# Optimization experiments

Measured on AMD Instinct MI355X. Metric: run time of the kernel, lower is better.

Reference implementation:

```python
import jax, jax.numpy as jnp
import numpy as np

H, D_MODEL, TOPK = 8, 512, 32
D_K = D_MODEL // H


def setup_inputs() -> dict:
    key = jax.random.key(0)
    ks = jax.random.split(key, 12)
    B, LQ, LM = 8, 1024, 4096
    s = 1.0 / np.sqrt(D_MODEL)
    inp = {
        "query": jax.random.normal(ks[0], (B, LQ, D_MODEL), jnp.float32),
        "key": jax.random.normal(ks[1], (B, LM, D_MODEL), jnp.float32),
        "value": jax.random.normal(ks[2], (B, LM, D_MODEL), jnp.float32),
        "Wq": jax.random.normal(ks[3], (D_MODEL, D_MODEL), jnp.float32) * s,
        "bq": jax.random.normal(ks[4], (D_MODEL,), jnp.float32) * s,
        "Wk": jax.random.normal(ks[5], (D_MODEL, D_MODEL), jnp.float32) * s,
        "bk": jax.random.normal(ks[6], (D_MODEL,), jnp.float32) * s,
        "Wv": jax.random.normal(ks[7], (D_MODEL, D_MODEL), jnp.float32) * s,
        "bv": jax.random.normal(ks[8], (D_MODEL,), jnp.float32) * s,
        "Wo": jax.random.normal(ks[9], (D_MODEL, D_MODEL), jnp.float32) * s,
        "bo": jax.random.normal(ks[10], (D_MODEL,), jnp.float32) * s,
    }
    return inp


def reference(query, key, value, Wq, bq, Wk, bk, Wv, bv, Wo, bo):
    B, LQ, _ = query.shape
    LM = key.shape[1]
    # torch Linear: x @ W.T + b
    q = (query @ Wq.T + bq).reshape(B, LQ, H, D_K).transpose(0, 2, 1, 3)  # [B,H,LQ,Dk]
    k = (key @ Wk.T + bk).reshape(B, LM, H, D_K).transpose(0, 2, 1, 3)    # [B,H,LM,Dk]
    v = (value @ Wv.T + bv).reshape(B, LM, H, D_K).transpose(0, 2, 1, 3)  # [B,H,LM,Dk]

    scores = jnp.einsum("bhqd,bhmd->bhqm", q, k) / np.sqrt(D_K)          # [B,H,LQ,LM]
    sel_scores, idx = jax.lax.top_k(scores, TOPK)                          # [B,H,LQ,TOPK]
    # gather selected values: [B,H,LQ,TOPK,Dk]
    sel_v = jnp.take_along_axis(v[:, :, None, :, :], idx[..., None], axis=3)
    p_attn = jax.nn.softmax(sel_scores, axis=-1)                           # dropout: eval mode
    x = jnp.einsum("bhqt,bhqtd->bhqd", p_attn, sel_v)                      # [B,H,LQ,Dk]
    x = x.transpose(0, 2, 1, 3).reshape(B, LQ, H * D_K)
    return x @ Wo.T + bo
```

## Files before the change

kernel.cpp:

```cpp
#include <hip/hip_runtime.h>
#include <math.h>

#define DEV static __device__ __forceinline__

DEV void load8(const float* p, float* v) {
    float4 a = *(const float4*)p;
    float4 b = *(const float4*)(p + 4);
    v[0] = a.x; v[1] = a.y; v[2] = a.z; v[3] = a.w;
    v[4] = b.x; v[5] = b.y; v[6] = b.z; v[7] = b.w;
}

DEV void gemm_body(const float* __restrict__ A, const float* __restrict__ W,
                   const float* __restrict__ bias, float* __restrict__ C,
                   int bm, int bn, int tid,
                   float (*As)[68], float (*Bs)[68])
{
    constexpr int BK = 32, NK = 512;
    const int tx = tid & 15, ty = tid >> 4;
    const int lr = tid >> 2, lk = (tid & 3) * 8;
    float acc[4][4] = {};

    for (int k0 = 0; k0 < NK; k0 += BK) {
        float va[8], vb[8];
        load8(A + (size_t)(bm + lr) * NK + k0 + lk, va);
        load8(W + (size_t)(bn + lr) * NK + k0 + lk, vb);
#pragma unroll
        for (int i = 0; i < 8; ++i) { As[lk + i][lr] = va[i]; Bs[lk + i][lr] = vb[i]; }
        __syncthreads();
#pragma unroll
        for (int kk = 0; kk < BK; ++kk) {
            float4 a4 = *(const float4*)&As[kk][ty * 4];
            float4 b4 = *(const float4*)&Bs[kk][tx * 4];
            float a[4] = {a4.x, a4.y, a4.z, a4.w};
            float b[4] = {b4.x, b4.y, b4.z, b4.w};
#pragma unroll
            for (int i = 0; i < 4; ++i)
#pragma unroll
                for (int j = 0; j < 4; ++j)
                    acc[i][j] = fmaf(a[i], b[j], acc[i][j]);
        }
        __syncthreads();
    }

    float4 bvv4 = *(const float4*)&bias[bn + tx * 4];
    float bvv[4] = {bvv4.x, bvv4.y, bvv4.z, bvv4.w};
#pragma unroll
    for (int i = 0; i < 4; ++i) {
        size_t row = (size_t)(bm + ty * 4 + i) * NK + bn + tx * 4;
        float4 o;
        o.x = acc[i][0] + bvv[0];
        o.y = acc[i][1] + bvv[1];
        o.z = acc[i][2] + bvv[2];
        o.w = acc[i][3] + bvv[3];
        *(float4*)&C[row] = o;
    }
}

__global__ __launch_bounds__(256) void gemm_nt512(
    const float* __restrict__ A, const float* __restrict__ W,
    const float* __restrict__ bias, float* __restrict__ C)
{
    __shared__ float As[32][68];
    __shared__ float Bs[32][68];
    gemm_body(A, W, bias, C, blockIdx.y * 64, blockIdx.x * 64, threadIdx.x, As, Bs);
}

__global__ __launch_bounds__(256) void gemm_qkv(
    const float* __restrict__ Aq, const float* __restrict__ Ak, const float* __restrict__ Av,
    const float* __restrict__ Wq, const float* __restrict__ Wk, const float* __restrict__ Wv,
    const float* __restrict__ bq, const float* __restrict__ bk, const float* __restrict__ bv,
    float* __restrict__ Cq, float* __restrict__ Ck, float* __restrict__ Cv)
{
    __shared__ float As[32][68];
    __shared__ float Bs[32][68];
    int yb = blockIdx.y;
    const float *A, *W, *bias; float* C; int bm;
    if (yb < 128)      { A = Aq; W = Wq; bias = bq; C = Cq; bm = yb * 64; }
    else if (yb < 640) { A = Ak; W = Wk; bias = bk; C = Ck; bm = (yb - 128) * 64; }
    else               { A = Av; W = Wv; bias = bv; C = Cv; bm = (yb - 640) * 64; }
    gemm_body(A, W, bias, C, bm, blockIdx.x * 64, threadIdx.x, As, Bs);
}

__global__ __launch_bounds__(256) void topk_attn_fused(
    const float* __restrict__ Qf, const float* __restrict__ Kf,
    const float* __restrict__ Vp, float* __restrict__ Xp,
    unsigned short* __restrict__ gbuf)
{
    constexpr int LQ = 1024, LM = 4096, DK = 64, D = 512, QT = 32, MT = 256, TK = 32, T = 24;
    constexpr int CAP = 624;
    __shared__ __align__(16) char smem[69632 + 8704 + 128];
    float (*ks)[68]   = (float (*)[68])(smem);
    float (*sc)[264]  = (float (*)[264])(smem + 34816);
    float (*wsel)[33] = (float (*)[33])(smem);
    int   (*isel)[33] = (int   (*)[33])(smem + 4224);
    float (*qs)[68]   = (float (*)[68])(smem + 69632);
    int*  cnt         = (int*)(smem + 69632 + 8704);

    const int tid  = threadIdx.x;
    const int lane = tid & 63;
    const int w    = tid >> 6;
    const int g    = lane >> 3, j = lane & 7;
    const int r    = 8 * w + g;
    const int qt = blockIdx.x, h = blockIdx.y, b = blockIdx.z;

    const size_t bb = ((size_t)(((b * 8) + h) * 32 + qt) * 32 + r) * CAP;

    {
        int rr = tid >> 3, d0 = (tid & 7) * 8;
        const float* src = Qf + ((size_t)(b * LQ + qt * QT + rr) * D + h * DK + d0);
        float4 a = *(const float4*)src;
        float4 c = *(const float4*)(src + 4);
        *(float4*)&qs[rr][d0]     = a;
        *(float4*)&qs[rr][d0 + 4] = c;
    }
    if (tid < 32) cnt[tid] = 0;

    float s0 = -INFINITY, s1 = -INFINITY, s2 = -INFINITY, s3 = -INFINITY;
    float tau = -INFINITY;

    const int qy = tid >> 5, tx = tid & 31;
    const int srr = tid >> 2, sd0 = (tid & 3) * 16;
    __syncthreads();

#pragma unroll 1
    for (int mc = 0; mc < LM; mc += MT) {
#pragma unroll
        for (int p = 0; p < 4; ++p) {
            const float* src = Kf + ((size_t)(b * LM + mc + 64 * p + srr) * D + h * DK + sd0);
#pragma unroll
            for (int i2 = 0; i2 < 16; i2 += 4)
                *(float4*)&ks[64 * p + srr][sd0 + i2] = *(const float4*)(src + i2);
        }
        __syncthreads();

        float acc[4][8] = {};
#pragma unroll 2
        for (int dc = 0; dc < DK; dc += 4) {
            float4 qa[4], kb[8];
#pragma unroll
            for (int i = 0; i < 4; ++i) qa[i] = *(const float4*)&qs[qy + 8 * i][dc];
#pragma unroll
            for (int jj = 0; jj < 8; ++jj) kb[jj] = *(const float4*)&ks[tx + 32 * jj][dc];
#pragma unroll
            for (int i = 0; i < 4; ++i)
#pragma unroll
                for (int jj = 0; jj < 8; ++jj) {
                    acc[i][jj] = fmaf(qa[i].x, kb[jj].x, acc[i][jj]);
                    acc[i][jj] = fmaf(qa[i].y, kb[jj].y, acc[i][jj]);
                    acc[i][jj] = fmaf(qa[i].z, kb[jj].z, acc[i][jj]);
                    acc[i][jj] = fmaf(qa[i].w, kb[jj].w, acc[i][jj]);
                }
        }
        __syncthreads();

#pragma unroll
        for (int i = 0; i < 4; ++i)
#pragma unroll
            for (int jj = 0; jj < 8; ++jj)
                sc[qy + 8 * i][tx + 32 * jj] = acc[i][jj] * 0.125f;
        __syncthreads();

#pragma unroll 8
        for (int c = 0; c < 32; ++c) {
            float v = sc[r][8 * c + j];
            if (v > s3) {
                if (v > s0)      { s3 = s2; s2 = s1; s1 = s0; s0 = v; }
                else if (v > s1) { s3 = s2; s2 = s1; s1 = v; }
                else if (v > s2) { s3 = s2; s2 = v; }
                else             { s3 = v; }
            }
            if (v > tau) {
                int pos = atomicAdd(&cnt[r], 1);
                if (pos < CAP) gbuf[bb + pos] = (unsigned short)(mc + 8 * c + j);
            }
            if ((c & 7) == 7) {
                float t4 = s3;
                t4 = fminf(t4, __shfl_xor(t4, 1));
                t4 = fminf(t4, __shfl_xor(t4, 2));
                t4 = fminf(t4, __shfl_xor(t4, 4));
                tau = t4;
            }
        }
        __syncthreads();
    }

    const int nc = min(cnt[r], CAP);
    float bv[T]; int bi[T];
#pragma unroll
    for (int t = 0; t < T; ++t) { bv[t] = -INFINITY; bi[t] = 0; }
    float curmin = -INFINITY; int minpos = 0, minidx = 0;

#pragma unroll 1
    for (int p = j; p < nc; p += 8) {
        int idx = gbuf[bb + p];
        const float* krow = Kf + ((size_t)(b * LM + idx) * D + h * DK);
        float a = 0.0f;
#pragma unroll
        for (int d = 0; d < DK; d += 4) {
            float4 k4 = *(const float4*)(krow + d);
            float4 q4 = *(const float4*)&qs[r][d];
            a = fmaf(q4.x, k4.x, a);
            a = fmaf(q4.y, k4.y, a);
            a = fmaf(q4.z, k4.z, a);
            a = fmaf(q4.w, k4.w, a);
        }
        float v = a * 0.125f;

        bool take = (v > curmin) || (v == curmin && idx < minidx);
        if (take) {
#pragma unroll
            for (int t = 0; t < T; ++t)
                if (t == minpos) { bv[t] = v; bi[t] = idx; }
            float mv = bv[0]; int mp = 0, mi = bi[0];
#pragma unroll
            for (int t = 1; t < T; ++t)
                if (bv[t] < mv || (bv[t] == mv && bi[t] > mi)) { mv = bv[t]; mp = t; mi = bi[t]; }
            curmin = mv; minpos = mp; minidx = mi;
        }
    }

    unsigned cons = 0;
    float m0 = 0.0f;
    double sum_part = 0.0;
#pragma unroll 1
    for (int t32 = 0; t32 < TK; ++t32) {
        float lm = -INFINITY; int li = 0x7fffffff; int lp = -1;
#pragma unroll
        for (int t = 0; t < T; ++t) {
            bool ok = !(cons & (1u << t));
            if (ok && (bv[t] > lm || (bv[t] == lm && bi[t] < li))) {
                lm = bv[t]; li = bi[t]; lp = t;
            }
        }
        float gv = lm; int gi = li;
#pragma unroll
        for (int k = 1; k < 8; k <<= 1) {
            float ov = __shfl_xor(gv, k);
            int   oi = __shfl_xor(gi, k);
            if (ov > gv || (ov == gv && oi < gi)) { gv = ov; gi = oi; }
        }
        if (lp >= 0 && gv == lm && gi == li) cons |= 1u << lp;
        if (t32 == 0) m0 = gv;
        if ((t32 & 7) == j) {
            double e = exp((double)(gv - m0));
            sum_part += e;
            isel[r][t32] = gi;
            wsel[r][t32] = (float)e;
        }
    }
#pragma unroll
    for (int k = 1; k < 8; k <<= 1) sum_part += __shfl_xor(sum_part, k);
    {
        double inv = 1.0 / sum_part;
#pragma unroll
        for (int tt = 0; tt < 4; ++tt) {
            int t = 8 * tt + j;
            wsel[r][t] = (float)((double)wsel[r][t] * inv);
        }
    }
    __syncthreads();

    {
        int rr = tid >> 3, d0 = (tid & 7) * 8;
        float4 a0 = {0, 0, 0, 0}, a1 = {0, 0, 0, 0};
#pragma unroll 1
        for (int t = 0; t < TK; ++t) {
            float ww = wsel[rr][t];
            int mi   = isel[rr][t];
            const float* vp = Vp + ((size_t)(b * LM + mi) * D + h * DK + d0);
            float4 v0 = *(const float4*)vp;
            float4 v1 = *(const float4*)(vp + 4);
            a0.x = fmaf(ww, v0.x, a0.x); a0.y = fmaf(ww, v0.y, a0.y);
            a0.z = fmaf(ww, v0.z, a0.z); a0.w = fmaf(ww, v0.w, a0.w);
            a1.x = fmaf(ww, v1.x, a1.x); a1.y = fmaf(ww, v1.y, a1.y);
            a1.z = fmaf(ww, v1.z, a1.z); a1.w = fmaf(ww, v1.w, a1.w);
        }
        float* xp = Xp + ((size_t)(b * LQ + qt * QT + rr) * D + h * DK + d0);
        *(float4*)xp       = a0;
        *(float4*)(xp + 4) = a1;
    }
}

extern "C" void kernel_launch(void* const* d_in, const int* in_sizes, int n_in,
                              void* d_out, int out_size, void* d_ws, size_t ws_size,
                              hipStream_t stream) {
    const float* query = (const float*)d_in[0];
    const float* key   = (const float*)d_in[1];
    const float* value = (const float*)d_in[2];
    const float* Wq    = (const float*)d_in[3];
    const float* bq    = (const float*)d_in[4];
    const float* Wk    = (const float*)d_in[5];
    const float* bk    = (const float*)d_in[6];
    const float* Wv    = (const float*)d_in[7];
    const float* bv    = (const float*)d_in[8];
    const float* Wo    = (const float*)d_in[9];
    const float* bo    = (const float*)d_in[10];
    float* out = (float*)d_out;

    float* Vp = (float*)d_ws;
    float* Xp = Vp + (size_t)32768 * 512;
    float* Qf = Xp + (size_t)8192 * 512;
    float* Kf = Qf + (size_t)8192 * 512;
    unsigned short* gbuf = (unsigned short*)((char*)d_ws + (size_t)167772160);

    dim3 blk(256);
    gemm_qkv<<<dim3(8, 1152), blk, 0, stream>>>(query, key, value,
                                                Wq, Wk, Wv, bq, bk, bv,
                                                Qf, Kf, Vp);
    topk_attn_fused<<<dim3(32, 8, 8), blk, 0, stream>>>(Qf, Kf, Vp, Xp, gbuf);
    gemm_nt512<<<dim3(8, 128), blk, 0, stream>>>(Xp, Wo, bo, out);
}
```

Before: 2.410 ms.

## Filter candidates directly from registers with per-row threshold and incremental top-24 merge

The score tile shrinks from 256 to 128 keys. Each thread now keeps a running top-2 per row in registers, and a row-wide minimum of those values sets a threshold used to push (score, index) pairs straight into a global pool. This removes the shared-memory score staging and the later recomputation of dot products against gathered K rows. The pool is merged into a per-lane top-24 whenever it fills past a threshold, which cuts pool capacity and shared memory use. In exchange it adds extra barriers and global writes of float2 entries, and relies on the 2-per-thread threshold staying loose enough for candidates to fit in the capacity.

After: 2.564 ms. 1.06x slower.

```diff
diff --git a/kernel.cpp b/kernel.cpp
--- a/kernel.cpp
+++ b/kernel.cpp
@@ -81,20 +81,36 @@
     gemm_body(A, W, bias, C, bm, blockIdx.x * 64, threadIdx.x, As, Bs);
 }
 
+template <int T>
+DEV void top24_insert(float v, int idx, float* bv, int* bi,
+                      float& curmin, int& minpos, int& minidx)
+{
+    bool take = (v > curmin) || (v == curmin && idx < minidx);
+    if (take) {
+#pragma unroll
+        for (int t = 0; t < T; ++t)
+            if (t == minpos) { bv[t] = v; bi[t] = idx; }
+        float mv = bv[0]; int mp = 0, mi = bi[0];
+#pragma unroll
+        for (int t = 1; t < T; ++t)
+            if (bv[t] < mv || (bv[t] == mv && bi[t] > mi)) { mv = bv[t]; mp = t; mi = bi[t]; }
+        curmin = mv; minpos = mp; minidx = mi;
+    }
+}
+
 __global__ __launch_bounds__(256) void topk_attn_fused(
     const float* __restrict__ Qf, const float* __restrict__ Kf,
     const float* __restrict__ Vp, float* __restrict__ Xp,
-    unsigned short* __restrict__ gbuf)
-{
-    constexpr int LQ = 1024, LM = 4096, DK = 64, D = 512, QT = 32, MT = 256, TK = 32, T = 24;
-    constexpr int CAP = 624;
-    __shared__ __align__(16) char smem[69632 + 8704 + 128];
+    float2* __restrict__ gpool)
+{
+    constexpr int LQ = 1024, LM = 4096, DK = 64, D = 512, QT = 32, MT = 128, TK = 32, T = 24;
+    constexpr int CAP = 160, THR = CAP - 128;
+    __shared__ __align__(16) char smem[34816 + 8704 + 128];
     float (*ks)[68]   = (float (*)[68])(smem);
-    float (*sc)[264]  = (float (*)[264])(smem + 34816);
     float (*wsel)[33] = (float (*)[33])(smem);
     int   (*isel)[33] = (int   (*)[33])(smem + 4224);
-    float (*qs)[68]   = (float (*)[68])(smem + 69632);
-    int*  cnt         = (int*)(smem + 69632 + 8704);
+    float (*qs)[68]   = (float (*)[68])(smem + 34816);
+    int*  cnt         = (int*)(smem + 34816 + 8704);
 
     const int tid  = threadIdx.x;
     const int lane = tid & 63;
@@ -103,7 +119,7 @@
     const int r    = 8 * w + g;
     const int qt = blockIdx.x, h = blockIdx.y, b = blockIdx.z;
 
-    const size_t bb = ((size_t)(((b * 8) + h) * 32 + qt) * 32 + r) * CAP;
+    const size_t bb = (size_t)(((b * 8 + h) * 32 + qt) * 32) * CAP;
 
     {
         int rr = tid >> 3, d0 = (tid & 7) * 8;
@@ -115,8 +131,14 @@
     }
     if (tid < 32) cnt[tid] = 0;
 
-    float s0 = -INFINITY, s1 = -INFINITY, s2 = -INFINITY, s3 = -INFINITY;
-    float tau = -INFINITY;
+    float bv[T]; int bi[T];
+#pragma unroll
+    for (int t = 0; t < T; ++t) { bv[t] = -INFINITY; bi[t] = 0; }
+    float curmin = -INFINITY; int minpos = 0, minidx = 0;
+
+    float s0[4], s1[4], tau[4];
+#pragma unroll
+    for (int i = 0; i < 4; ++i) { s0[i] = -INFINITY; s1[i] = -INFINITY; tau[i] = -INFINITY; }
 
     const int qy = tid >> 5, tx = tid & 31;
     const int srr = tid >> 2, sd0 = (tid & 3) * 16;
@@ -125,7 +147,7 @@
 #pragma unroll 1
     for (int mc = 0; mc < LM; mc += MT) {
 #pragma unroll
-        for (int p = 0; p < 4; ++p) {
+        for (int p = 0; p < 2; ++p) {
             const float* src = Kf + ((size_t)(b * LM + mc + 64 * p + srr) * D + h * DK + sd0);
 #pragma unroll
             for (int i2 = 0; i2 < 16; i2 += 4)
@@ -133,89 +155,83 @@
         }
         __syncthreads();
 
-        float acc[4][8] = {};
+        float acc[4][4] = {};
 #pragma unroll 2
         for (int dc = 0; dc < DK; dc += 4) {
-            float4 qa[4], kb[8];
+            float4 qa[4], kb[4];
 #pragma unroll
             for (int i = 0; i < 4; ++i) qa[i] = *(const float4*)&qs[qy + 8 * i][dc];
 #pragma unroll
-            for (int jj = 0; jj < 8; ++jj) kb[jj] = *(const float4*)&ks[tx + 32 * jj][dc];
+            for (int jj = 0; jj < 4; ++jj) kb[jj] = *(const float4*)&ks[tx + 32 * jj][dc];
 #pragma unroll
             for (int i = 0; i < 4; ++i)
 #pragma unroll
-                for (int jj = 0; jj < 8; ++jj) {
+                for (int jj = 0; jj < 4; ++jj) {
                     acc[i][jj] = fmaf(qa[i].x, kb[jj].x, acc[i][jj]);
                     acc[i][jj] = fmaf(qa[i].y, kb[jj].y, acc[i][jj]);
                     acc[i][jj] = fmaf(qa[i].z, kb[jj].z, acc[i][jj]);
                     acc[i][jj] = fmaf(qa[i].w, kb[jj].w, acc[i][jj]);
                 }
         }
+
+#pragma unroll
+        for (int i = 0; i < 4; ++i)
+#pragma unroll
+            for (int jj = 0; jj < 4; ++jj) {
+                float v = acc[i][jj] * 0.125f;
+                acc[i][jj] = v;
+                if (v > s1[i]) {
+                    if (v > s0[i]) { s1[i] = s0[i]; s0[i] = v; }
+                    else           { s1[i] = v; }
+                }
+            }
+
+#pragma unroll
+        for (int i = 0; i < 4; ++i) {
+            float t4 = s1[i];
+            t4 = fminf(t4, __shfl_xor(t4, 1));
+            t4 = fminf(t4, __shfl_xor(t4, 2));
+            t4 = fminf(t4, __shfl_xor(t4, 4));
+            t4 = fminf(t4, __shfl_xor(t4, 8));
+            t4 = fminf(t4, __shfl_xor(t4, 16));
+            tau[i] = t4;
+        }
+
+#pragma unroll
+        for (int i = 0; i < 4; ++i) {
+            int row = qy + 8 * i;
+#pragma unroll
+            for (int jj = 0; jj < 4; ++jj) {
+                float v = acc[i][jj];
+                if (v >= tau[i]) {
+                    int pos = atomicAdd(&cnt[row], 1);
+                    if (pos < CAP)
+                        gpool[bb + (size_t)row * CAP + pos] =
+                            make_float2(v, __int_as_float(mc + tx + 32 * jj));
+                }
+            }
+        }
         __syncthreads();
 
-#pragma unroll
-        for (int i = 0; i < 4; ++i)
-#pragma unroll
-            for (int jj = 0; jj < 8; ++jj)
-                sc[qy + 8 * i][tx + 32 * jj] = acc[i][jj] * 0.125f;
-        __syncthreads();
-
-#pragma unroll 8
-        for (int c = 0; c < 32; ++c) {
-            float v = sc[r][8 * c + j];
-            if (v > s3) {
-                if (v > s0)      { s3 = s2; s2 = s1; s1 = s0; s0 = v; }
-                else if (v > s1) { s3 = s2; s2 = s1; s1 = v; }
-                else if (v > s2) { s3 = s2; s2 = v; }
-                else             { s3 = v; }
+        {
+            int nc = min(cnt[r], CAP);
+            if (nc > THR) {
+#pragma unroll 1
+                for (int p = j; p < nc; p += 8) {
+                    float2 e = gpool[bb + (size_t)r * CAP + p];
+                    top24_insert<T>(e.x, __float_as_int(e.y), bv, bi, curmin, minpos, minidx);
+                }
+                if (j == 0) cnt[r] = 0;
             }
-            if (v > tau) {
-                int pos = atomicAdd(&cnt[r], 1);
-                if (pos < CAP) gbuf[bb + pos] = (unsigned short)(mc + 8 * c + j);
-            }
-            if ((c & 7) == 7) {
-                float t4 = s3;
-                t4 = fminf(t4, __shfl_xor(t4, 1));
-                t4 = fminf(t4, __shfl_xor(t4, 2));
-                t4 = fminf(t4, __shfl_xor(t4, 4));
-                tau = t4;
-            }
-        }
-        __syncthreads();
-    }
-
-    const int nc = min(cnt[r], CAP);
-    float bv[T]; int bi[T];
-#pragma unroll
-    for (int t = 0; t < T; ++t) { bv[t] = -INFINITY; bi[t] = 0; }
-    float curmin = -INFINITY; int minpos = 0, minidx = 0;
-
-#pragma unroll 1
-    for (int p = j; p < nc; p += 8) {
-        int idx = gbuf[bb + p];
-        const float* krow = Kf + ((size_t)(b * LM + idx) * D + h * DK);
-        float a = 0.0f;
-#pragma unroll
-        for (int d = 0; d < DK; d += 4) {
-            float4 k4 = *(const float4*)(krow + d);
-            float4 q4 = *(const float4*)&qs[r][d];
-            a = fmaf(q4.x, k4.x, a);
-            a = fmaf(q4.y, k4.y, a);
-            a = fmaf(q4.z, k4.z, a);
-            a = fmaf(q4.w, k4.w, a);
-        }
-        float v = a * 0.125f;
-
-        bool take = (v > curmin) || (v == curmin && idx < minidx);
-        if (take) {
-#pragma unroll
-            for (int t = 0; t < T; ++t)
-                if (t == minpos) { bv[t] = v; bi[t] = idx; }
-            float mv = bv[0]; int mp = 0, mi = bi[0];
-#pragma unroll
-            for (int t = 1; t < T; ++t)
-                if (bv[t] < mv || (bv[t] == mv && bi[t] > mi)) { mv = bv[t]; mp = t; mi = bi[t]; }
-            curmin = mv; minpos = mp; minidx = mi;
+        }
+    }
+
+    {
+        int nc = min(cnt[r], CAP);
+#pragma unroll 1
+        for (int p = j; p < nc; p += 8) {
+            float2 e = gpool[bb + (size_t)r * CAP + p];
+            top24_insert<T>(e.x, __float_as_int(e.y), bv, bi, curmin, minpos, minidx);
         }
     }
 
@@ -301,12 +317,12 @@
     float* Xp = Vp + (size_t)32768 * 512;
     float* Qf = Xp + (size_t)8192 * 512;
     float* Kf = Qf + (size_t)8192 * 512;
-    unsigned short* gbuf = (unsigned short*)((char*)d_ws + (size_t)167772160);
+    float2* gpool = (float2*)((char*)d_ws + (size_t)167772160);
 
     dim3 blk(256);
     gemm_qkv<<<dim3(8, 1152), blk, 0, stream>>>(query, key, value,
                                                 Wq, Wk, Wv, bq, bk, bv,
                                                 Qf, Kf, Vp);
-    topk_attn_fused<<<dim3(32, 8, 8), blk, 0, stream>>>(Qf, Kf, Vp, Xp, gbuf);
+    topk_attn_fused<<<dim3(32, 8, 8), blk, 0, stream>>>(Qf, Kf, Vp, Xp, gpool);
     gemm_nt512<<<dim3(8, 128), blk, 0, stream>>>(Xp, Wo, bo, out);
 }
```

## Replace candidate-buffer top-k with in-register streaming top-24 and swizzle K tile

Applied to the files above, without the earlier changes.

Drops the two-pass top-k, which wrote threshold-passing indices to a global buffer through shared-memory atomics and then recomputed those dot products from global K. Each lane now keeps its own register top-24 list and updates it straight from the shared-memory score tile on every chunk. It also XOR-swizzles the column layout of the K tile in shared memory to cut bank conflicts in the QK^T inner loop. The cost is a full 24-entry min rescan per accepted candidate inside a fully unrolled loop, which adds register pressure and divergence. The tie-break on equal scores no longer considers the index.

Result: no change. 2.457 ms (+1.9%).

```diff
diff --git a/kernel.cpp b/kernel.cpp
--- a/kernel.cpp
+++ b/kernel.cpp
@@ -83,18 +83,15 @@
 
 __global__ __launch_bounds__(256) void topk_attn_fused(
     const float* __restrict__ Qf, const float* __restrict__ Kf,
-    const float* __restrict__ Vp, float* __restrict__ Xp,
-    unsigned short* __restrict__ gbuf)
+    const float* __restrict__ Vp, float* __restrict__ Xp)
 {
     constexpr int LQ = 1024, LM = 4096, DK = 64, D = 512, QT = 32, MT = 256, TK = 32, T = 24;
-    constexpr int CAP = 624;
-    __shared__ __align__(16) char smem[69632 + 8704 + 128];
+    __shared__ __align__(16) char smem[69632 + 8704];
     float (*ks)[68]   = (float (*)[68])(smem);
     float (*sc)[264]  = (float (*)[264])(smem + 34816);
     float (*wsel)[33] = (float (*)[33])(smem);
     int   (*isel)[33] = (int   (*)[33])(smem + 4224);
     float (*qs)[68]   = (float (*)[68])(smem + 69632);
-    int*  cnt         = (int*)(smem + 69632 + 8704);
 
     const int tid  = threadIdx.x;
     const int lane = tid & 63;
@@ -102,8 +99,6 @@
     const int g    = lane >> 3, j = lane & 7;
     const int r    = 8 * w + g;
     const int qt = blockIdx.x, h = blockIdx.y, b = blockIdx.z;
-
-    const size_t bb = ((size_t)(((b * 8) + h) * 32 + qt) * 32 + r) * CAP;
 
     {
         int rr = tid >> 3, d0 = (tid & 7) * 8;
@@ -113,13 +108,16 @@
         *(float4*)&qs[rr][d0]     = a;
         *(float4*)&qs[rr][d0 + 4] = c;
     }
-    if (tid < 32) cnt[tid] = 0;
-
-    float s0 = -INFINITY, s1 = -INFINITY, s2 = -INFINITY, s3 = -INFINITY;
-    float tau = -INFINITY;
+
+    float bv[T]; int bi[T];
+#pragma unroll
+    for (int t = 0; t < T; ++t) { bv[t] = -INFINITY; bi[t] = 0; }
+    float curmin = -INFINITY; int minpos = 0;
 
     const int qy = tid >> 5, tx = tid & 31;
     const int srr = tid >> 2, sd0 = (tid & 3) * 16;
+    const int dxw = (srr >> 3) & 3;
+    const int dxr = (tx >> 3) & 3;
     __syncthreads();
 
 #pragma unroll 1
@@ -127,20 +125,24 @@
 #pragma unroll
         for (int p = 0; p < 4; ++p) {
             const float* src = Kf + ((size_t)(b * LM + mc + 64 * p + srr) * D + h * DK + sd0);
-#pragma unroll
-            for (int i2 = 0; i2 < 16; i2 += 4)
-                *(float4*)&ks[64 * p + srr][sd0 + i2] = *(const float4*)(src + i2);
+            int row = 64 * p + srr;
+#pragma unroll
+            for (int i2 = 0; i2 < 16; i2 += 4) {
+                int c = (sd0 + i2) >> 2;
+                *(float4*)&ks[row][(c ^ dxw) << 2] = *(const float4*)(src + i2);
+            }
         }
         __syncthreads();
 
         float acc[4][8] = {};
 #pragma unroll 2
         for (int dc = 0; dc < DK; dc += 4) {
+            int col = (((dc >> 2) ^ dxr) << 2);
             float4 qa[4], kb[8];
 #pragma unroll
             for (int i = 0; i < 4; ++i) qa[i] = *(const float4*)&qs[qy + 8 * i][dc];
 #pragma unroll
-            for (int jj = 0; jj < 8; ++jj) kb[jj] = *(const float4*)&ks[tx + 32 * jj][dc];
+            for (int jj = 0; jj < 8; ++jj) kb[jj] = *(const float4*)&ks[tx + 32 * jj][col];
 #pragma unroll
             for (int i = 0; i < 4; ++i)
 #pragma unroll
@@ -160,63 +162,22 @@
                 sc[qy + 8 * i][tx + 32 * jj] = acc[i][jj] * 0.125f;
         __syncthreads();
 
-#pragma unroll 8
+#pragma unroll
         for (int c = 0; c < 32; ++c) {
             float v = sc[r][8 * c + j];
-            if (v > s3) {
-                if (v > s0)      { s3 = s2; s2 = s1; s1 = s0; s0 = v; }
-                else if (v > s1) { s3 = s2; s2 = s1; s1 = v; }
-                else if (v > s2) { s3 = s2; s2 = v; }
-                else             { s3 = v; }
+            if (v > curmin) {
+                int idx = mc + 8 * c + j;
+#pragma unroll
+                for (int t = 0; t < T; ++t)
+                    if (t == minpos) { bv[t] = v; bi[t] = idx; }
+                float mv = bv[0]; int mp = 0;
+#pragma unroll
+                for (int t = 1; t < T; ++t)
+                    if (bv[t] < mv) { mv = bv[t]; mp = t; }
+                curmin = mv; minpos = mp;
             }
-            if (v > tau) {
-                int pos = atomicAdd(&cnt[r], 1);
-                if (pos < CAP) gbuf[bb + pos] = (unsigned short)(mc + 8 * c + j);
-            }
-            if ((c & 7) == 7) {
-                float t4 = s3;
-                t4 = fminf(t4, __shfl_xor(t4, 1));
-                t4 = fminf(t4, __shfl_xor(t4, 2));
-                t4 = fminf(t4, __shfl_xor(t4, 4));
-                tau = t4;
-            }
-        }
-        __syncthreads();
-    }
-
-    const int nc = min(cnt[r], CAP);
-    float bv[T]; int bi[T];
-#pragma unroll
-    for (int t = 0; t < T; ++t) { bv[t] = -INFINITY; bi[t] = 0; }
-    float curmin = -INFINITY; int minpos = 0, minidx = 0;
-
-#pragma unroll 1
-    for (int p = j; p < nc; p += 8) {
-        int idx = gbuf[bb + p];
-        const float* krow = Kf + ((size_t)(b * LM + idx) * D + h * DK);
-        float a = 0.0f;
-#pragma unroll
-        for (int d = 0; d < DK; d += 4) {
-            float4 k4 = *(const float4*)(krow + d);
-            float4 q4 = *(const float4*)&qs[r][d];
-            a = fmaf(q4.x, k4.x, a);
-            a = fmaf(q4.y, k4.y, a);
-            a = fmaf(q4.z, k4.z, a);
-            a = fmaf(q4.w, k4.w, a);
-        }
-        float v = a * 0.125f;
-
-        bool take = (v > curmin) || (v == curmin && idx < minidx);
-        if (take) {
-#pragma unroll
-            for (int t = 0; t < T; ++t)
-                if (t == minpos) { bv[t] = v; bi[t] = idx; }
-            float mv = bv[0]; int mp = 0, mi = bi[0];
-#pragma unroll
-            for (int t = 1; t < T; ++t)
-                if (bv[t] < mv || (bv[t] == mv && bi[t] > mi)) { mv = bv[t]; mp = t; mi = bi[t]; }
-            curmin = mv; minpos = mp; minidx = mi;
-        }
+        }
+        __syncthreads();
     }
 
     unsigned cons = 0;
@@ -301,12 +262,11 @@
     float* Xp = Vp + (size_t)32768 * 512;
     float* Qf = Xp + (size_t)8192 * 512;
     float* Kf = Qf + (size_t)8192 * 512;
-    unsigned short* gbuf = (unsigned short*)((char*)d_ws + (size_t)167772160);
 
     dim3 blk(256);
     gemm_qkv<<<dim3(8, 1152), blk, 0, stream>>>(query, key, value,
                                                 Wq, Wk, Wv, bq, bk, bv,
                                                 Qf, Kf, Vp);
-    topk_attn_fused<<<dim3(32, 8, 8), blk, 0, stream>>>(Qf, Kf, Vp, Xp, gbuf);
+    topk_attn_fused<<<dim3(32, 8, 8), blk, 0, stream>>>(Qf, Kf, Vp, Xp);
     gemm_nt512<<<dim3(8, 128), blk, 0, stream>>>(Xp, Wo, bo, out);
 }
```
